# Kernel optimization log

Measured on AMD Instinct MI355X. Metric: run time of the kernel, lower is better.

## Reference

```python
import jax, jax.numpy as jnp
import numpy as np


def ste_sign(x):
    # Forward: sign(x); backward: identity (straight-through estimator).
    return jax.lax.stop_gradient(jnp.sign(x) - x) + x


def setup_inputs() -> dict:
    key = jax.random.key(0)
    k1, k2 = jax.random.split(key)
    x = jax.random.normal(k1, (8192, 4096), dtype=jnp.float32)
    weight = jax.random.normal(k2, (4096, 4096), dtype=jnp.float32) * 0.02
    return {"x": x, "weight": weight}


def reference(x, weight):
    # binary_linear: sign(x) @ sign(weight).T  (F.linear semantics)
    x_bin = ste_sign(x)          # [N, in]
    w_bin = ste_sign(weight)     # [out, in]
    return jnp.einsum('ni,oi->no', x_bin, w_bin)
```

## Files before the change

kernel.cpp:

```cpp
#include <hip/hip_runtime.h>
#include <hip/hip_bf16.h>
#include <stdint.h>

typedef int i32x4 __attribute__((ext_vector_type(4)));
typedef int i32x8 __attribute__((ext_vector_type(8)));
typedef float f32x4 __attribute__((ext_vector_type(4)));

__device__ __forceinline__ unsigned int sign_nib(float x) {
  return x > 0.0f ? 0x2u : (x < 0.0f ? 0xAu : 0x0u);
}

__device__ __forceinline__ unsigned short pack4(const float4& a) {
  return (unsigned short)(sign_nib(a.x)
                        | (sign_nib(a.y) << 4)
                        | (sign_nib(a.z) << 8)
                        | (sign_nib(a.w) << 12));
}

__global__ __launch_bounds__(256)
void binarize_fp4_v3(const float* __restrict__ x,
                     const float* __restrict__ w,
                     unsigned short* __restrict__ xb,
                     unsigned short* __restrict__ wb,
                     int bx) {
  const float4* src;
  unsigned short* dst;
  int b = blockIdx.x;
  if (b < bx) { src = (const float4*)x; dst = xb; }
  else        { src = (const float4*)w; dst = wb; b -= bx; }

  const size_t base = (size_t)b * 1024 + threadIdx.x;
  float4 v0 = src[base];
  float4 v1 = src[base + 256];
  float4 v2 = src[base + 512];
  float4 v3 = src[base + 768];

  dst[base]       = pack4(v0);
  dst[base + 256] = pack4(v1);
  dst[base + 512] = pack4(v2);
  dst[base + 768] = pack4(v3);
}

__device__ __forceinline__ void load_lds16(const void* g, void* l) {
  __builtin_amdgcn_global_load_lds(
      (const __attribute__((address_space(1))) void*)g,
      (__attribute__((address_space(3))) void*)l,
      16, 0, 0);
}

__device__ __forceinline__ void bar() {
  asm volatile("s_barrier" ::: "memory");
}
template <int N>
__device__ __forceinline__ void waitvm() {
  asm volatile("s_waitcnt vmcnt(%0)" ::"i"(N) : "memory");
}

__device__ __forceinline__ i32x8 rd8(const char* p) {
  i32x4 q = *(const i32x4*)p;
  return __builtin_shufflevector(q, q, 0, 1, 2, 3, -1, -1, -1, -1);
}

__global__ __launch_bounds__(512, 2)
void gemm_bt_fp4(const unsigned char* __restrict__ A,
                 const unsigned char* __restrict__ B,
                 float* __restrict__ C,
                 int M, int N, int K, int nbn) {
  constexpr int BM = 256, BN = 256;
  __shared__ __attribute__((aligned(16))) char lds[4 * 32768];

  int nwg = gridDim.x;
  int bid = blockIdx.x;
  int cpx = nwg >> 3;
  int swz = (bid & 7) * cpx + (bid >> 3);
  int tm = swz / nbn;
  int tn = swz % nbn;

  const int t = threadIdx.x;
  const int lane = t & 63;
  const int wid = t >> 6;
  const int wm = wid >> 2;
  const int wn = wid & 3;
  const int lrow = lane & 15;
  const int kg = lane >> 4;

  const int Kb = K >> 1;
  const size_t rowA0 = (size_t)tm * BM;
  const size_t rowB0 = (size_t)tn * BN;

  f32x4 acc[8][4] = {};

  const int nt = K / 128;

  const int soff0 = wid * 1024 + lane * 16;
  const int srow0 = soff0 >> 6;
  const int scb0 = ((soff0 >> 4) & 3) ^ ((srow0 >> 1) & 3);
  const int soff1 = 8192 + wid * 1024 + lane * 16;
  const int srow1 = soff1 >> 6;
  const int scb1 = ((soff1 >> 4) & 3) ^ ((srow1 >> 1) & 3);

  auto stage = [&](int tt) {
    const int b = tt & 3;
    const int k0b = tt * 64;
    load_lds16(A + (rowA0 + srow0) * Kb + k0b + scb0 * 16,
               lds + b * 32768 + wid * 1024);
    load_lds16(A + (rowA0 + srow1) * Kb + k0b + scb1 * 16,
               lds + b * 32768 + 8192 + wid * 1024);
    load_lds16(B + (rowB0 + srow0) * Kb + k0b + scb0 * 16,
               lds + b * 32768 + 16384 + wid * 1024);
    load_lds16(B + (rowB0 + srow1) * Kb + k0b + scb1 * 16,
               lds + b * 32768 + 16384 + 8192 + wid * 1024);
  };

  const int rcol = ((kg ^ ((lrow >> 1) & 3)) << 4);
  const int aoff = (wm * 128 + lrow) * 64 + rcol;
  const int boff = 16384 + (wn * 64 + lrow) * 64 + rcol;

  const int SC = 0x7F7F7F7F;

  stage(0); stage(1);

  for (int tt = 0; tt < nt; ++tt) {
    const int b = tt & 3;
    if (tt + 1 < nt) waitvm<4>(); else waitvm<0>();
    bar();

    const char* Ab = lds + b * 32768 + aoff;
    const char* Bb = lds + b * 32768 + boff;

    i32x8 bf[4], af[4];
    #pragma unroll
    for (int n = 0; n < 4; ++n)
      bf[n] = rd8(Bb + n * 1024);
    #pragma unroll
    for (int m = 0; m < 4; ++m)
      af[m] = rd8(Ab + m * 1024);

    if (tt + 2 < nt) stage(tt + 2);

    #pragma unroll
    for (int m = 0; m < 4; ++m)
      #pragma unroll
      for (int n = 0; n < 4; ++n)
        acc[m][n] = __builtin_amdgcn_mfma_scale_f32_16x16x128_f8f6f4(
            af[m], bf[n], acc[m][n], 4, 4, 0, SC, 0, SC);

    i32x8 ag[4];
    #pragma unroll
    for (int m = 0; m < 4; ++m)
      ag[m] = rd8(Ab + (m + 4) * 1024);

    #pragma unroll
    for (int m = 0; m < 4; ++m)
      #pragma unroll
      for (int n = 0; n < 4; ++n)
        acc[m + 4][n] = __builtin_amdgcn_mfma_scale_f32_16x16x128_f8f6f4(
            ag[m], bf[n], acc[m + 4][n], 4, 4, 0, SC, 0, SC);
  }

  const size_t cRow0 = rowA0 + (size_t)wm * 128;
  const size_t cCol0 = rowB0 + (size_t)wn * 64;
  const int orow = kg * 4;
  #pragma unroll
  for (int m = 0; m < 8; ++m)
    #pragma unroll
    for (int n = 0; n < 4; ++n)
      #pragma unroll
      for (int r = 0; r < 4; ++r)
        C[(cRow0 + m * 16 + orow + r) * N + cCol0 + n * 16 + lrow] =
            acc[m][n][r];
}

extern "C" void kernel_launch(void* const* d_in, const int* in_sizes, int n_in,
                              void* d_out, int out_size, void* d_ws, size_t ws_size,
                              hipStream_t stream) {
  const float* x = (const float*)d_in[0];
  const float* w = (const float*)d_in[1];
  float* out = (float*)d_out;

  const int K = 4096;
  const int M = in_sizes[0] / K;
  const int N = in_sizes[1] / K;

  unsigned char* xb = (unsigned char*)d_ws;
  unsigned char* wb = xb + (size_t)M * (K / 2);

  int bxx = (M * K) / 4096;
  int bxw = (N * K) / 4096;
  binarize_fp4_v3<<<dim3(bxx + bxw), dim3(256), 0, stream>>>(
      x, w, (unsigned short*)xb, (unsigned short*)wb, bxx);

  int nbm = M / 256;
  int nbn = N / 256;
  gemm_bt_fp4<<<dim3(nbm * nbn), dim3(512), 0, stream>>>(
      xb, wb, out, M, N, K, nbn);
}
```

Measured before the change: 119.8 us.

## Switch FP4 GEMM inner loop to 32x32x64 scaled MFMA tiles

Replaces the 16x16x128 FP4 scaled MFMA with the 32x32x64 variant. Each wave now computes its 128x64 tile as 4x2 fragments of 32x32, each accumulating two K-halves, instead of 8x4 fragments of 16x16. LDS reads are remapped to the new operand layout and the C store is rewritten for the 32x32 accumulator layout. The aim is fewer MFMA issues and fewer LDS fragment loads per tile. The risk is different instruction latency and dependency chains, since two consecutive MFMAs now write the same accumulator.

```diff
diff --git a/kernel.cpp b/kernel.cpp
--- a/kernel.cpp
+++ b/kernel.cpp
@@ -4,7 +4,7 @@
 
 typedef int i32x4 __attribute__((ext_vector_type(4)));
 typedef int i32x8 __attribute__((ext_vector_type(8)));
-typedef float f32x4 __attribute__((ext_vector_type(4)));
+typedef float f32x16 __attribute__((ext_vector_type(16)));
 
 __device__ __forceinline__ unsigned int sign_nib(float x) {
   return x > 0.0f ? 0x2u : (x < 0.0f ? 0xAu : 0x0u);
@@ -81,14 +81,14 @@
   const int wid = t >> 6;
   const int wm = wid >> 2;
   const int wn = wid & 3;
-  const int lrow = lane & 15;
-  const int kg = lane >> 4;
+  const int l31 = lane & 31;
+  const int h = lane >> 5;
 
   const int Kb = K >> 1;
   const size_t rowA0 = (size_t)tm * BM;
   const size_t rowB0 = (size_t)tn * BN;
 
-  f32x4 acc[8][4] = {};
+  f32x16 acc[4][2] = {};
 
   const int nt = K / 128;
 
@@ -112,9 +112,9 @@
                lds + b * 32768 + 16384 + 8192 + wid * 1024);
   };
 
-  const int rcol = ((kg ^ ((lrow >> 1) & 3)) << 4);
-  const int aoff = (wm * 128 + lrow) * 64 + rcol;
-  const int boff = 16384 + (wn * 64 + lrow) * 64 + rcol;
+  const int rp = (l31 >> 1) & 3;
+  const int pc0 = ((h ^ rp) << 4);
+  const int pc1 = (((2 + h) ^ rp) << 4);
 
   const int SC = 0x7F7F7F7F;
 
@@ -125,50 +125,53 @@
     if (tt + 1 < nt) waitvm<4>(); else waitvm<0>();
     bar();
 
-    const char* Ab = lds + b * 32768 + aoff;
-    const char* Bb = lds + b * 32768 + boff;
-
-    i32x8 bf[4], af[4];
-    #pragma unroll
-    for (int n = 0; n < 4; ++n)
-      bf[n] = rd8(Bb + n * 1024);
-    #pragma unroll
-    for (int m = 0; m < 4; ++m)
-      af[m] = rd8(Ab + m * 1024);
+    const char* Ab = lds + b * 32768 + (wm * 128 + l31) * 64;
+    const char* Bb = lds + b * 32768 + 16384 + (wn * 64 + l31) * 64;
+
+    i32x8 bf[2][2], af[4];
+    #pragma unroll
+    for (int nf = 0; nf < 2; ++nf) {
+      bf[nf][0] = rd8(Bb + nf * 2048 + pc0);
+      bf[nf][1] = rd8(Bb + nf * 2048 + pc1);
+    }
+    #pragma unroll
+    for (int mf = 0; mf < 4; ++mf)
+      af[mf] = rd8(Ab + mf * 2048 + pc0);
 
     if (tt + 2 < nt) stage(tt + 2);
 
     #pragma unroll
-    for (int m = 0; m < 4; ++m)
+    for (int mf = 0; mf < 4; ++mf)
       #pragma unroll
-      for (int n = 0; n < 4; ++n)
-        acc[m][n] = __builtin_amdgcn_mfma_scale_f32_16x16x128_f8f6f4(
-            af[m], bf[n], acc[m][n], 4, 4, 0, SC, 0, SC);
+      for (int nf = 0; nf < 2; ++nf)
+        acc[mf][nf] = __builtin_amdgcn_mfma_scale_f32_32x32x64_f8f6f4(
+            af[mf], bf[nf][0], acc[mf][nf], 4, 4, 0, SC, 0, SC);
 
     i32x8 ag[4];
     #pragma unroll
-    for (int m = 0; m < 4; ++m)
-      ag[m] = rd8(Ab + (m + 4) * 1024);
-
-    #pragma unroll
-    for (int m = 0; m < 4; ++m)
+    for (int mf = 0; mf < 4; ++mf)
+      ag[mf] = rd8(Ab + mf * 2048 + pc1);
+
+    #pragma unroll
+    for (int mf = 0; mf < 4; ++mf)
       #pragma unroll
-      for (int n = 0; n < 4; ++n)
-        acc[m + 4][n] = __builtin_amdgcn_mfma_scale_f32_16x16x128_f8f6f4(
-            ag[m], bf[n], acc[m + 4][n], 4, 4, 0, SC, 0, SC);
+      for (int nf = 0; nf < 2; ++nf)
+        acc[mf][nf] = __builtin_amdgcn_mfma_scale_f32_32x32x64_f8f6f4(
+            ag[mf], bf[nf][1], acc[mf][nf], 4, 4, 0, SC, 0, SC);
   }
 
   const size_t cRow0 = rowA0 + (size_t)wm * 128;
   const size_t cCol0 = rowB0 + (size_t)wn * 64;
-  const int orow = kg * 4;
   #pragma unroll
-  for (int m = 0; m < 8; ++m)
-    #pragma unroll
-    for (int n = 0; n < 4; ++n)
+  for (int mf = 0; mf < 4; ++mf)
+    #pragma unroll
+    for (int nf = 0; nf < 2; ++nf)
       #pragma unroll
-      for (int r = 0; r < 4; ++r)
-        C[(cRow0 + m * 16 + orow + r) * N + cCol0 + n * 16 + lrow] =
-            acc[m][n][r];
+      for (int r = 0; r < 16; ++r) {
+        const int row = (r & 3) + 8 * (r >> 2) + 4 * h;
+        C[(cRow0 + mf * 32 + row) * N + cCol0 + nf * 32 + l31] =
+            acc[mf][nf][r];
+      }
 }
 
 extern "C" void kernel_launch(void* const* d_in, const int* in_sizes, int n_in,
```

Measured after the change: 124.9 us. +4.2%, slower.

## Prefetch next tile's A fragments into double-buffered registers ahead of MFMAs

Applied to the files above, without the earlier changes.

Restructures the main loop into a two-step unrolled body with ping-pong register arrays for A fragments. The A fragments for the next K tile are loaded from LDS while the current tile's MFMAs run. All 32 MFMAs then issue as one block behind a scheduling barrier. This targets LDS read latency stalls between MFMA groups, at the cost of doubled A-fragment registers (more VGPR pressure) and a stricter waitvm<0> every iteration that may expose global load latency.

```diff
diff --git a/kernel.cpp b/kernel.cpp
--- a/kernel.cpp
+++ b/kernel.cpp
@@ -48,9 +48,6 @@
       16, 0, 0);
 }
 
-__device__ __forceinline__ void bar() {
-  asm volatile("s_barrier" ::: "memory");
-}
 template <int N>
 __device__ __forceinline__ void waitvm() {
   asm volatile("s_waitcnt vmcnt(%0)" ::"i"(N) : "memory");
@@ -118,44 +115,46 @@
 
   const int SC = 0x7F7F7F7F;
 
+  i32x8 afA[8], afB[8];
+
   stage(0); stage(1);
+  waitvm<4>();
+  __builtin_amdgcn_s_barrier();
+  {
+    const char* Ab = lds + aoff;
+    #pragma unroll
+    for (int m = 0; m < 8; ++m)
+      afA[m] = rd8(Ab + m * 1024);
+  }
 
-  for (int tt = 0; tt < nt; ++tt) {
+  auto body = [&](i32x8 (&afC)[8], i32x8 (&afN)[8], int tt) {
+    waitvm<0>();
+    __builtin_amdgcn_s_barrier();
     const int b = tt & 3;
-    if (tt + 1 < nt) waitvm<4>(); else waitvm<0>();
-    bar();
-
-    const char* Ab = lds + b * 32768 + aoff;
     const char* Bb = lds + b * 32768 + boff;
-
-    i32x8 bf[4], af[4];
+    i32x8 bf[4];
     #pragma unroll
     for (int n = 0; n < 4; ++n)
       bf[n] = rd8(Bb + n * 1024);
+    if (tt + 1 < nt) {
+      const char* Ab = lds + ((tt + 1) & 3) * 32768 + aoff;
+      #pragma unroll
+      for (int m = 0; m < 8; ++m)
+        afN[m] = rd8(Ab + m * 1024);
+    }
+    if (tt + 2 < nt) stage(tt + 2);
+    __builtin_amdgcn_sched_barrier(0);
     #pragma unroll
-    for (int m = 0; m < 4; ++m)
-      af[m] = rd8(Ab + m * 1024);
-
-    if (tt + 2 < nt) stage(tt + 2);
-
-    #pragma unroll
-    for (int m = 0; m < 4; ++m)
+    for (int m = 0; m < 8; ++m)
       #pragma unroll
       for (int n = 0; n < 4; ++n)
         acc[m][n] = __builtin_amdgcn_mfma_scale_f32_16x16x128_f8f6f4(
-            af[m], bf[n], acc[m][n], 4, 4, 0, SC, 0, SC);
+            afC[m], bf[n], acc[m][n], 4, 4, 0, SC, 0, SC);
+  };
 
-    i32x8 ag[4];
-    #pragma unroll
-    for (int m = 0; m < 4; ++m)
-      ag[m] = rd8(Ab + (m + 4) * 1024);
-
-    #pragma unroll
-    for (int m = 0; m < 4; ++m)
-      #pragma unroll
-      for (int n = 0; n < 4; ++n)
-        acc[m + 4][n] = __builtin_amdgcn_mfma_scale_f32_16x16x128_f8f6f4(
-            ag[m], bf[n], acc[m + 4][n], 4, 4, 0, SC, 0, SC);
+  for (int tt = 0; tt < nt; tt += 2) {
+    body(afA, afB, tt);
+    body(afB, afA, tt + 1);
   }
 
   const size_t cRow0 = rowA0 + (size_t)wm * 128;
```

After: 222.5 us. 85.7% more time.
